# Kernel tuning notes

Hardware: AMD Instinct MI355X
Metric: run time of the kernel (lower is better)

Reference implementation:

```python
import jax, jax.numpy as jnp
import numpy as np
import math

B, S, H, HKV, DH = 2, 2048, 32, 1, 128  # batch, seq, q heads, kv heads, per-head/model dim
D_K = 128


def setup_inputs() -> dict:
    key = jax.random.key(0)
    ks = jax.random.split(key, 11)
    sc = 0.02
    return {
        "query": jax.random.normal(ks[0], (B, S, DH), jnp.float32),
        "key": jax.random.normal(ks[1], (B, S, DH), jnp.float32),
        "values": jax.random.normal(ks[2], (B, S, DH), jnp.float32),
        "W_q": jax.random.normal(ks[3], (DH, H * DH), jnp.float32) * sc,
        "b_q": jnp.zeros((H * DH,), jnp.float32),
        "W_k": jax.random.normal(ks[4], (DH, HKV * DH), jnp.float32) * sc,
        "b_k": jnp.zeros((HKV * DH,), jnp.float32),
        "W_v": jax.random.normal(ks[5], (DH, HKV * DH), jnp.float32) * sc,
        "b_v": jnp.zeros((HKV * DH,), jnp.float32),
        "W_o": jax.random.normal(ks[6], (H * DH, DH), jnp.float32) * sc,
        "b_o": jnp.zeros((DH,), jnp.float32),
    }


def reference(query, key, values, W_q, b_q, W_k, b_k, W_v, b_v, W_o, b_o):
    # Projections (note: the original uses raw .view(-1, H, S, DH), which we
    # replicate exactly — it is a reshape, not a transpose).
    q = (query @ W_q + b_q).reshape(-1, H, S, DH)      # [B,H,S,DH]
    k = (key @ W_k + b_k).reshape(-1, HKV, S, DH)       # [B,1,S,DH]
    v = (values @ W_v + b_v).reshape(-1, HKV, S, DH)    # [B,1,S,DH]

    # RoPE outputs in the original forward are computed but never used
    # (dead code), and mask defaults to None -> no masking. Dropout omitted
    # for deterministic reference.
    scores = jnp.matmul(q, jnp.swapaxes(k, -1, -2)) / math.sqrt(D_K)  # [B,H,S,S]
    attn = jax.nn.softmax(scores, axis=-1)
    out = jnp.matmul(attn, v)                           # [B,H,S,DH]
    out = jnp.swapaxes(out, 1, 2).reshape(-1, S, H * DH)
    return out @ W_o + b_o                              # [B,S,DH]
```

## Files before the change

### kernel.cpp

```cpp
#include <hip/hip_runtime.h>
#include <hip/hip_bf16.h>
#include <math.h>


typedef __hip_bfloat16 bf16;
typedef __attribute__((ext_vector_type(8))) short short8;
typedef __attribute__((ext_vector_type(4))) float floatx4;

static constexpr int B_ = 2;
static constexpr int S_ = 2048;
static constexpr int H_ = 32;
static constexpr int DH_ = 128;

#define GL16(gp, lp)                                              \
  __builtin_amdgcn_global_load_lds(                               \
      (const __attribute__((address_space(1))) void*)(gp),        \
      (__attribute__((address_space(3))) void*)(lp), 16, 0, 0)

__global__ void detect_dtype(const unsigned short* __restrict__ q,
                             int* __restrict__ flag) {
  int t = threadIdx.x;
  int cnt = 0;
#pragma unroll
  for (int i = 0; i < 8; ++i) {
    unsigned short u = q[t * 8 + i];
    int e = (u >> 7) & 0xFF;
    if (e < 0x60) cnt++;
  }
#pragma unroll
  for (int off = 1; off < 64; off <<= 1) cnt += __shfl_xor(cnt, off);
  if (t == 0) *flag = (cnt >= 8) ? 1 : 0;
}

__global__ void cvt3_bf16(const void* __restrict__ a, const void* __restrict__ b,
                          const void* __restrict__ c, bf16* __restrict__ da,
                          bf16* __restrict__ db, bf16* __restrict__ dc, int n,
                          const int* __restrict__ flag) {
  int i = blockIdx.x * 256 + threadIdx.x;
  if (i >= n) return;
  const void* s = (blockIdx.y == 0) ? a : (blockIdx.y == 1) ? b : c;
  bf16* d = (blockIdx.y == 0) ? da : (blockIdx.y == 1) ? db : dc;
  d[i] = (*flag) ? __float2bfloat16(((const float*)s)[i]) : ((const bf16*)s)[i];
}

__global__ void cvt_biases(const void* __restrict__ bq, const void* __restrict__ bk,
                           const void* __restrict__ bv, const void* __restrict__ bo,
                           float* __restrict__ fq, float* __restrict__ fk,
                           float* __restrict__ fv, float* __restrict__ fo,
                           const int* __restrict__ flag, float qscale) {
  int i = blockIdx.x * 256 + threadIdx.x;
  const void* s;
  float* d;
  int off;
  float sc = 1.f;
  if (i < 4096) { s = bq; d = fq; off = i; sc = qscale; }
  else if (i < 4224) { s = bk; d = fk; off = i - 4096; }
  else if (i < 4352) { s = bv; d = fv; off = i - 4224; }
  else if (i < 4480) { s = bo; d = fo; off = i - 4352; }
  else return;
  float v = (*flag) ? ((const float*)s)[off]
                    : __bfloat162float(((const bf16*)s)[off]);
  d[off] = v * sc;
}

__global__ void ttranspose(const void* __restrict__ W, bf16* __restrict__ Wt,
                           int K, int N, const int* __restrict__ flag,
                           float scale) {
  __shared__ bf16 tile[64][66];
  int n0 = blockIdx.x * 64, k0 = blockIdx.y * 64;
  int c = threadIdx.x & 63;
  int r4 = threadIdx.x >> 6;
  bool f = (*flag) != 0;
#pragma unroll
  for (int i = 0; i < 16; ++i) {
    int r = r4 * 16 + i;
    float v = f ? ((const float*)W)[(size_t)(k0 + r) * N + n0 + c]
                : __bfloat162float(((const bf16*)W)[(size_t)(k0 + r) * N + n0 + c]);
    tile[r][c] = __float2bfloat16(v * scale);
  }
  __syncthreads();
#pragma unroll
  for (int i = 0; i < 16; ++i) {
    int cc = r4 * 16 + i;
    Wt[(size_t)(n0 + cc) * K + k0 + c] = tile[c][cc];
  }
}

template <int MODE>
__global__ __launch_bounds__(256) void gemm2(
    const bf16* __restrict__ A, int lda, const bf16* __restrict__ Bt, int ldb,
    const float* __restrict__ bias, bf16* __restrict__ Cb,
    float* __restrict__ Cf, int K_len, int ldc) {
  const int lane = threadIdx.x & 63;
  const int wave = threadIdx.x >> 6;
  const int lm = lane & 15;
  const int quad = lane >> 4;
  const int row_base = blockIdx.y * 64 + wave * 16;
  const int col_base = blockIdx.x * 64;
  const int koff = blockIdx.z * K_len;

  const bf16* arow = A + (size_t)(row_base + lm) * lda + koff + quad * 8;
  const bf16* brow = Bt + (size_t)(col_base + lm) * ldb + koff + quad * 8;

  floatx4 z = {0.f, 0.f, 0.f, 0.f};
  floatx4 acc[4] = {z, z, z, z};

  for (int kk = 0; kk < K_len; kk += 32) {
    short8 a = *(const short8*)(arow + kk);
#pragma unroll
    for (int t = 0; t < 4; ++t) {
      short8 b = *(const short8*)(brow + (size_t)(t * 16) * ldb + kk);
      acc[t] = __builtin_amdgcn_mfma_f32_16x16x32_bf16(a, b, acc[t], 0, 0, 0);
    }
  }

#pragma unroll
  for (int t = 0; t < 4; ++t) {
    int col = col_base + t * 16 + lm;
#pragma unroll
    for (int r = 0; r < 4; ++r) {
      int row = row_base + quad * 4 + r;
      if (MODE == 0) {
        Cb[(size_t)row * ldc + col] = __float2bfloat16(acc[t][r] + bias[col]);
      } else if (MODE == 3) {
        Cb[((size_t)((row >> 11) * DH_ + col)) * S_ + (row & 2047)] =
            __float2bfloat16(acc[t][r] + bias[col]);
      } else {
        Cf[(size_t)blockIdx.z * (4096 * 128) + (size_t)row * ldc + col] =
            acc[t][r];
      }
    }
  }
}

__global__ void finish_out(const float* __restrict__ parts,
                           const float* __restrict__ bias,
                           float* __restrict__ out) {
  int i = blockIdx.x * 256 + threadIdx.x;
  const float4* p = (const float4*)parts;
  float4 a = p[i];
  float4 b = p[i + 131072];
  float4 c = p[i + 262144];
  float4 d = p[i + 393216];
  float4 bb = ((const float4*)bias)[i & 31];
  float4 o;
  o.x = a.x + b.x + c.x + d.x + bb.x;
  o.y = a.y + b.y + c.y + d.y + bb.y;
  o.z = a.z + b.z + c.z + d.z + bb.z;
  o.w = a.w + b.w + c.w + d.w + bb.w;
  ((float4*)out)[i] = o;
}

static __device__ __forceinline__ unsigned bpack(float lo, float hi) {
  unsigned a = __float_as_uint(lo) + 0x8000u;
  unsigned b = __float_as_uint(hi) + 0x8000u;
  return __builtin_amdgcn_perm(b, a, 0x07060302u);
}

static __device__ __forceinline__ float fexp2(float x) {
#if __has_builtin(__builtin_amdgcn_exp2f)
  return __builtin_amdgcn_exp2f(x);
#else
  return exp2f(x);
#endif
}

static __device__ __forceinline__ void pexchange(const unsigned pk[8],
                                                 int quad, short8* pf) {
  const bool q0 = (quad & 1);
  unsigned sA0 = q0 ? pk[0] : pk[2];
  unsigned sA1 = q0 ? pk[1] : pk[3];
  unsigned sA2 = q0 ? pk[4] : pk[6];
  unsigned sA3 = q0 ? pk[5] : pk[7];
  unsigned r0 = (unsigned)__shfl_xor((int)sA0, 16);
  unsigned r1 = (unsigned)__shfl_xor((int)sA1, 16);
  unsigned r2 = (unsigned)__shfl_xor((int)sA2, 16);
  unsigned r3 = (unsigned)__shfl_xor((int)sA3, 16);
  unsigned M0 = q0 ? r0 : pk[0];
  unsigned M1 = q0 ? r1 : pk[1];
  unsigned M2 = q0 ? pk[2] : r0;
  unsigned M3 = q0 ? pk[3] : r1;
  unsigned M4 = q0 ? r2 : pk[4];
  unsigned M5 = q0 ? r3 : pk[5];
  unsigned M6 = q0 ? pk[6] : r2;
  unsigned M7 = q0 ? pk[7] : r3;
  const bool swp = (quad == 1) || (quad == 2);
  union { unsigned u[4]; short8 v; } f0, f1;
  unsigned t0, t1;
  t0 = (unsigned)__shfl_xor((int)M0, 48); f0.u[0] = swp ? t0 : M0;
  t1 = (unsigned)__shfl_xor((int)M1, 48); f0.u[1] = swp ? t1 : M1;
  t0 = (unsigned)__shfl_xor((int)M2, 48); f0.u[2] = swp ? t0 : M2;
  t1 = (unsigned)__shfl_xor((int)M3, 48); f0.u[3] = swp ? t1 : M3;
  t0 = (unsigned)__shfl_xor((int)M4, 48); f1.u[0] = swp ? t0 : M4;
  t1 = (unsigned)__shfl_xor((int)M5, 48); f1.u[1] = swp ? t1 : M5;
  t0 = (unsigned)__shfl_xor((int)M6, 48); f1.u[2] = swp ? t0 : M6;
  t1 = (unsigned)__shfl_xor((int)M7, 48); f1.u[3] = swp ? t1 : M7;
  pf[0] = f0.v;
  pf[1] = f1.v;
}

__global__ __launch_bounds__(256, 2) void flash_attn(
    const bf16* __restrict__ Qp, const bf16* __restrict__ Kp,
    const bf16* __restrict__ Vt, bf16* __restrict__ O2c) {
  const int tid = threadIdx.x;
  const int lane = tid & 63;
  const int wave = tid >> 6;
  const int lm = lane & 15;
  const int quad = lane >> 4;
  const int qt = blockIdx.x;
  const int h = blockIdx.y;
  const int b = blockIdx.z;

  __shared__ __align__(16) bf16 Klds[2][64 * 128];
  __shared__ __align__(16) bf16 Vlds[2][128 * 64];

  const int base = qt * 128 + wave * 32;
  const bf16* qrow = Qp + ((size_t)b * S_ + h * 64 + (base >> 5)) * 4096;
  short8 qf0[4], qf1[4];
#pragma unroll
  for (int ks = 0; ks < 4; ++ks) {
    qf0[ks] = *(const short8*)(qrow + lm * 128 + quad * 8 + ks * 32);
    qf1[ks] = *(const short8*)(qrow + (16 + lm) * 128 + quad * 8 + ks * 32);
  }

  const bf16* Kb = Kp + (size_t)b * S_ * DH_;
  const bf16* Vb = Vt + (size_t)b * DH_ * S_;
  const int sw = lm & 7;

  const bf16* kgp[4];
  const bf16* vgp[4];
#pragma unroll
  for (int i = 0; i < 4; ++i) {
    const int inst = wave * 4 + i;
    const int krow = inst * 4 + quad;
    kgp[i] = Kb + (size_t)krow * 128 + ((lm ^ (krow & 7)) * 8);
    const int vrow = inst * 8 + (lane >> 3);
    vgp[i] = Vb + (size_t)vrow * S_ + (((lane & 7) ^ (vrow & 7)) * 8);
  }

  floatx4 z = {0.f, 0.f, 0.f, 0.f};
  floatx4 oa0[8], oa1[8];
#pragma unroll
  for (int nt = 0; nt < 8; ++nt) { oa0[nt] = z; oa1[nt] = z; }
  float ls0 = 0.f, ls1 = 0.f;

#pragma unroll
  for (int i = 0; i < 4; ++i) {
    GL16(kgp[i], &Klds[0][(wave * 4 + i) * 512]);
    GL16(vgp[i], &Vlds[0][(wave * 4 + i) * 512]);
    kgp[i] += 64 * 128;
    vgp[i] += 64;
  }
  __syncthreads();

  int cur = 0;
  for (int kb = 0; kb < S_; kb += 64) {
    const bf16* Kc = Klds[cur];
    const bf16* Vc = Vlds[cur];
    if (kb + 64 < S_) {
      bf16* Kn = Klds[cur ^ 1];
      bf16* Vn = Vlds[cur ^ 1];
#pragma unroll
      for (int i = 0; i < 4; ++i) {
        GL16(kgp[i], Kn + (wave * 4 + i) * 512);
        GL16(vgp[i], Vn + (wave * 4 + i) * 512);
        kgp[i] += 64 * 128;
        vgp[i] += 64;
      }
    }

    floatx4 s0[4] = {z, z, z, z}, s1[4] = {z, z, z, z};
    __builtin_amdgcn_s_setprio(1);
#pragma unroll
    for (int t = 0; t < 4; ++t) {
#pragma unroll
      for (int ks = 0; ks < 4; ++ks) {
        short8 kf = *(const short8*)(&Kc[(t * 16 + lm) * 128 +
                                         (((quad + 4 * ks) ^ sw) * 8)]);
        s0[t] = __builtin_amdgcn_mfma_f32_16x16x32_bf16(kf, qf0[ks], s0[t],
                                                        0, 0, 0);
        s1[t] = __builtin_amdgcn_mfma_f32_16x16x32_bf16(kf, qf1[ks], s1[t],
                                                        0, 0, 0);
      }
    }
    __builtin_amdgcn_s_setprio(0);

    unsigned pk0[8], pk1[8];
#pragma unroll
    for (int t = 0; t < 4; ++t) {
      float a0 = fexp2(s0[t][0]), a1 = fexp2(s0[t][1]);
      float a2 = fexp2(s0[t][2]), a3 = fexp2(s0[t][3]);
      ls0 += (a0 + a1) + (a2 + a3);
      pk0[2 * t] = bpack(a0, a1);
      pk0[2 * t + 1] = bpack(a2, a3);
      float c0 = fexp2(s1[t][0]), c1 = fexp2(s1[t][1]);
      float c2 = fexp2(s1[t][2]), c3 = fexp2(s1[t][3]);
      ls1 += (c0 + c1) + (c2 + c3);
      pk1[2 * t] = bpack(c0, c1);
      pk1[2 * t + 1] = bpack(c2, c3);
    }
    short8 pf0[2], pf1[2];
    pexchange(pk0, quad, pf0);
    pexchange(pk1, quad, pf1);

    __builtin_amdgcn_s_setprio(1);
#pragma unroll
    for (int ks2 = 0; ks2 < 2; ++ks2) {
#pragma unroll
      for (int nt = 0; nt < 8; ++nt) {
        short8 vf = *(const short8*)(&Vc[(nt * 16 + lm) * 64 +
                                         (((quad + 4 * ks2) ^ sw) * 8)]);
        oa0[nt] = __builtin_amdgcn_mfma_f32_16x16x32_bf16(pf0[ks2], vf,
                                                          oa0[nt], 0, 0, 0);
        oa1[nt] = __builtin_amdgcn_mfma_f32_16x16x32_bf16(pf1[ks2], vf,
                                                          oa1[nt], 0, 0, 0);
      }
    }
    __builtin_amdgcn_s_setprio(0);
    __syncthreads();
    cur ^= 1;
  }

  ls0 += __shfl_xor(ls0, 16);
  ls0 += __shfl_xor(ls0, 32);
  ls1 += __shfl_xor(ls1, 16);
  ls1 += __shfl_xor(ls1, 32);
  float inv0[4], inv1[4];
#pragma unroll
  for (int r = 0; r < 4; ++r) {
    inv0[r] = 1.0f / __shfl(ls0, quad * 4 + r);
    inv1[r] = 1.0f / __shfl(ls1, quad * 4 + r);
  }

#pragma unroll
  for (int r = 0; r < 4; ++r) {
    int s2a = base + quad * 4 + r;
    int s2b = s2a + 16;
    size_t ba = ((size_t)b * S_ + s2a) * 4096 + (size_t)h * 128;
    size_t bb = ((size_t)b * S_ + s2b) * 4096 + (size_t)h * 128;
#pragma unroll
    for (int nt = 0; nt < 8; ++nt) {
      O2c[ba + nt * 16 + lm] = __float2bfloat16(oa0[nt][r] * inv0[r]);
      O2c[bb + nt * 16 + lm] = __float2bfloat16(oa1[nt][r] * inv1[r]);
    }
  }
}

extern "C" void kernel_launch(void* const* d_in, const int* in_sizes, int n_in,
                              void* d_out, int out_size, void* d_ws,
                              size_t ws_size, hipStream_t stream) {
  (void)in_sizes;
  (void)n_in;
  (void)out_size;
  (void)ws_size;

  const void* query = d_in[0];
  const void* key = d_in[1];
  const void* values = d_in[2];
  const void* W_q = d_in[3];
  const void* b_q = d_in[4];
  const void* W_k = d_in[5];
  const void* b_k = d_in[6];
  const void* W_v = d_in[7];
  const void* b_v = d_in[8];
  const void* W_o = d_in[9];
  const void* b_o = d_in[10];
  float* out = (float*)d_out;

  const float kScale = 0.1275174388204085f;
  const int M = B_ * S_;
  const int QN = B_ * S_ * DH_;

  char* w = (char*)d_ws;
  auto carve = [&](size_t bytes) -> char* {
    char* p = w;
    w += (bytes + 255) & ~(size_t)255;
    return p;
  };
  int* flag = (int*)carve(4);
  bf16* cQ = (bf16*)carve((size_t)QN * 2);
  bf16* cK = (bf16*)carve((size_t)QN * 2);
  bf16* cV = (bf16*)carve((size_t)QN * 2);
  float* fbq = (float*)carve((size_t)H_ * DH_ * 4);
  float* fbk = (float*)carve((size_t)DH_ * 4);
  float* fbv = (float*)carve((size_t)DH_ * 4);
  float* fbo = (float*)carve((size_t)DH_ * 4);
  bf16* Wqt = (bf16*)carve((size_t)DH_ * H_ * DH_ * 2);
  bf16* Wkt = (bf16*)carve((size_t)DH_ * DH_ * 2);
  bf16* Wvt = (bf16*)carve((size_t)DH_ * DH_ * 2);
  bf16* Wot = (bf16*)carve((size_t)H_ * DH_ * DH_ * 2);
  bf16* Kp = (bf16*)carve((size_t)B_ * S_ * DH_ * 2);
  bf16* Vtp = (bf16*)carve((size_t)B_ * S_ * DH_ * 2);
  bf16* Qp = (bf16*)carve((size_t)M * H_ * DH_ * 2);
  bf16* O2c = (bf16*)carve((size_t)M * H_ * DH_ * 2);

  float* parts = (float*)Qp;

  detect_dtype<<<1, 64, 0, stream>>>((const unsigned short*)query, flag);
  cvt3_bf16<<<dim3(QN / 256, 3), 256, 0, stream>>>(query, key, values, cQ, cK,
                                                   cV, QN, flag);
  cvt_biases<<<18, 256, 0, stream>>>(b_q, b_k, b_v, b_o, fbq, fbk, fbv, fbo,
                                     flag, kScale);

  ttranspose<<<dim3(H_ * DH_ / 64, DH_ / 64), 256, 0, stream>>>(
      W_q, Wqt, DH_, H_ * DH_, flag, kScale);
  ttranspose<<<dim3(DH_ / 64, DH_ / 64), 256, 0, stream>>>(W_k, Wkt, DH_, DH_,
                                                           flag, 1.0f);
  ttranspose<<<dim3(DH_ / 64, DH_ / 64), 256, 0, stream>>>(W_v, Wvt, DH_, DH_,
                                                           flag, 1.0f);
  ttranspose<<<dim3(DH_ / 64, H_ * DH_ / 64), 256, 0, stream>>>(
      W_o, Wot, H_ * DH_, DH_, flag, 1.0f);

  gemm2<0><<<dim3(2, 64), 256, 0, stream>>>(cK, DH_, Wkt, DH_, fbk, Kp,
                                            nullptr, DH_, DH_);
  gemm2<3><<<dim3(2, 64), 256, 0, stream>>>(cV, DH_, Wvt, DH_, fbv, Vtp,
                                            nullptr, DH_, 0);
  gemm2<0><<<dim3(64, 64), 256, 0, stream>>>(cQ, DH_, Wqt, DH_, fbq, Qp,
                                             nullptr, DH_, H_ * DH_);

  flash_attn<<<dim3(S_ / 128, H_, B_), 256, 0, stream>>>(Qp, Kp, Vtp, O2c);

  gemm2<4><<<dim3(DH_ / 64, M / 64, 4), 256, 0, stream>>>(
      O2c, H_ * DH_, Wot, H_ * DH_, nullptr, nullptr, parts,
      (H_ * DH_) / 4, DH_);

  finish_out<<<QN / 4 / 256, 256, 0, stream>>>(parts, fbo, out);
}
```

Measured before the change: 363.5 us.

## Merge prep kernels, fuse QKV GEMMs, single-buffer LDS in flash attention

Fuses the conversion, bias and four weight-transpose kernels into one launch, and the three QKV projection GEMMs into one grid, to cut launch count and tail effects. In flash attention, the K/V double buffer becomes a single LDS buffer and launch bounds go from 2 to 4 blocks per CU to raise occupancy. The loads for the next tile are now issued only after compute finishes, so global-to-LDS transfers no longer overlap with MFMA work inside a block and must be hidden by the other resident blocks.

```diff
diff --git a/kernel.cpp b/kernel.cpp
--- a/kernel.cpp
+++ b/kernel.cpp
@@ -32,45 +32,13 @@
   if (t == 0) *flag = (cnt >= 8) ? 1 : 0;
 }
 
-__global__ void cvt3_bf16(const void* __restrict__ a, const void* __restrict__ b,
-                          const void* __restrict__ c, bf16* __restrict__ da,
-                          bf16* __restrict__ db, bf16* __restrict__ dc, int n,
-                          const int* __restrict__ flag) {
-  int i = blockIdx.x * 256 + threadIdx.x;
-  if (i >= n) return;
-  const void* s = (blockIdx.y == 0) ? a : (blockIdx.y == 1) ? b : c;
-  bf16* d = (blockIdx.y == 0) ? da : (blockIdx.y == 1) ? db : dc;
-  d[i] = (*flag) ? __float2bfloat16(((const float*)s)[i]) : ((const bf16*)s)[i];
-}
-
-__global__ void cvt_biases(const void* __restrict__ bq, const void* __restrict__ bk,
-                           const void* __restrict__ bv, const void* __restrict__ bo,
-                           float* __restrict__ fq, float* __restrict__ fk,
-                           float* __restrict__ fv, float* __restrict__ fo,
-                           const int* __restrict__ flag, float qscale) {
-  int i = blockIdx.x * 256 + threadIdx.x;
-  const void* s;
-  float* d;
-  int off;
-  float sc = 1.f;
-  if (i < 4096) { s = bq; d = fq; off = i; sc = qscale; }
-  else if (i < 4224) { s = bk; d = fk; off = i - 4096; }
-  else if (i < 4352) { s = bv; d = fv; off = i - 4224; }
-  else if (i < 4480) { s = bo; d = fo; off = i - 4352; }
-  else return;
-  float v = (*flag) ? ((const float*)s)[off]
-                    : __bfloat162float(((const bf16*)s)[off]);
-  d[off] = v * sc;
-}
-
-__global__ void ttranspose(const void* __restrict__ W, bf16* __restrict__ Wt,
-                           int K, int N, const int* __restrict__ flag,
-                           float scale) {
-  __shared__ bf16 tile[64][66];
-  int n0 = blockIdx.x * 64, k0 = blockIdx.y * 64;
+static __device__ void do_ttranspose(const void* __restrict__ W,
+                                     bf16* __restrict__ Wt, int K, int N,
+                                     bool f, float scale, int bx, int by,
+                                     bf16 (*tile)[66]) {
+  int n0 = bx * 64, k0 = by * 64;
   int c = threadIdx.x & 63;
   int r4 = threadIdx.x >> 6;
-  bool f = (*flag) != 0;
 #pragma unroll
   for (int i = 0; i < 16; ++i) {
     int r = r4 * 16 + i;
@@ -86,11 +54,106 @@
   }
 }
 
-template <int MODE>
-__global__ __launch_bounds__(256) void gemm2(
-    const bf16* __restrict__ A, int lda, const bf16* __restrict__ Bt, int ldb,
-    const float* __restrict__ bias, bf16* __restrict__ Cb,
-    float* __restrict__ Cf, int K_len, int ldc) {
+__global__ void prep(const void* __restrict__ query, const void* __restrict__ key,
+                     const void* __restrict__ values, bf16* __restrict__ cQ,
+                     bf16* __restrict__ cK, bf16* __restrict__ cV,
+                     const void* __restrict__ bq, const void* __restrict__ bk,
+                     const void* __restrict__ bv, const void* __restrict__ bo,
+                     float* __restrict__ fbq, float* __restrict__ fbk,
+                     float* __restrict__ fbv, float* __restrict__ fbo,
+                     const void* __restrict__ Wq, bf16* __restrict__ Wqt,
+                     const void* __restrict__ Wk, bf16* __restrict__ Wkt,
+                     const void* __restrict__ Wv, bf16* __restrict__ Wvt,
+                     const void* __restrict__ Wo, bf16* __restrict__ Wot,
+                     const int* __restrict__ flag, float qscale) {
+  __shared__ bf16 tile[64][66];
+  const int id = blockIdx.x;
+  const bool f = (*flag) != 0;
+  if (id < 6144) {
+    int y = id >> 11, x = id & 2047;
+    int i = x * 256 + threadIdx.x;
+    const void* s = (y == 0) ? query : (y == 1) ? key : values;
+    bf16* d = (y == 0) ? cQ : (y == 1) ? cK : cV;
+    d[i] = f ? __float2bfloat16(((const float*)s)[i]) : ((const bf16*)s)[i];
+  } else if (id < 6162) {
+    int i = (id - 6144) * 256 + threadIdx.x;
+    const void* s; float* d; int off; float sc = 1.f;
+    if (i < 4096) { s = bq; d = fbq; off = i; sc = qscale; }
+    else if (i < 4224) { s = bk; d = fbk; off = i - 4096; }
+    else if (i < 4352) { s = bv; d = fbv; off = i - 4224; }
+    else if (i < 4480) { s = bo; d = fbo; off = i - 4352; }
+    else return;
+    float v = f ? ((const float*)s)[off]
+                : __bfloat162float(((const bf16*)s)[off]);
+    d[off] = v * sc;
+  } else if (id < 6290) {
+    int j = id - 6162;
+    do_ttranspose(Wq, Wqt, DH_, H_ * DH_, f, qscale, j % 64, j / 64, tile);
+  } else if (id < 6294) {
+    int j = id - 6290;
+    do_ttranspose(Wk, Wkt, DH_, DH_, f, 1.0f, j % 2, j / 2, tile);
+  } else if (id < 6298) {
+    int j = id - 6294;
+    do_ttranspose(Wv, Wvt, DH_, DH_, f, 1.0f, j % 2, j / 2, tile);
+  } else {
+    int j = id - 6298;
+    do_ttranspose(Wo, Wot, H_ * DH_, DH_, f, 1.0f, j % 2, j / 2, tile);
+  }
+}
+
+__global__ __launch_bounds__(256) void gemm_qkv(
+    const bf16* __restrict__ cQ, const bf16* __restrict__ cK,
+    const bf16* __restrict__ cV, const bf16* __restrict__ Wqt,
+    const bf16* __restrict__ Wkt, const bf16* __restrict__ Wvt,
+    const float* __restrict__ fbq, const float* __restrict__ fbk,
+    const float* __restrict__ fbv, bf16* __restrict__ Qp,
+    bf16* __restrict__ Kp, bf16* __restrict__ Vtp) {
+  const int bx = blockIdx.x;
+  const bf16* A; const bf16* Bt; const float* bias; bf16* Cb;
+  int mode, ldc, colb;
+  if (bx < 64)      { A = cQ; Bt = Wqt; bias = fbq; Cb = Qp;  mode = 0; ldc = 4096; colb = bx; }
+  else if (bx < 66) { A = cK; Bt = Wkt; bias = fbk; Cb = Kp;  mode = 0; ldc = 128;  colb = bx - 64; }
+  else              { A = cV; Bt = Wvt; bias = fbv; Cb = Vtp; mode = 3; ldc = 0;    colb = bx - 66; }
+
+  const int lane = threadIdx.x & 63;
+  const int wave = threadIdx.x >> 6;
+  const int lm = lane & 15;
+  const int quad = lane >> 4;
+  const int row_base = blockIdx.y * 64 + wave * 16;
+  const int col_base = colb * 64;
+
+  const bf16* arow = A + (size_t)(row_base + lm) * DH_ + quad * 8;
+  const bf16* brow = Bt + (size_t)(col_base + lm) * DH_ + quad * 8;
+
+  floatx4 z = {0.f, 0.f, 0.f, 0.f};
+  floatx4 acc[4] = {z, z, z, z};
+  for (int kk = 0; kk < DH_; kk += 32) {
+    short8 a = *(const short8*)(arow + kk);
+#pragma unroll
+    for (int t = 0; t < 4; ++t) {
+      short8 b = *(const short8*)(brow + (size_t)(t * 16) * DH_ + kk);
+      acc[t] = __builtin_amdgcn_mfma_f32_16x16x32_bf16(a, b, acc[t], 0, 0, 0);
+    }
+  }
+#pragma unroll
+  for (int t = 0; t < 4; ++t) {
+    int col = col_base + t * 16 + lm;
+#pragma unroll
+    for (int r = 0; r < 4; ++r) {
+      int row = row_base + quad * 4 + r;
+      if (mode == 0) {
+        Cb[(size_t)row * ldc + col] = __float2bfloat16(acc[t][r] + bias[col]);
+      } else {
+        Cb[((size_t)((row >> 11) * DH_ + col)) * S_ + (row & 2047)] =
+            __float2bfloat16(acc[t][r] + bias[col]);
+      }
+    }
+  }
+}
+
+__global__ __launch_bounds__(256) void gemm_out(
+    const bf16* __restrict__ A, const bf16* __restrict__ Bt,
+    float* __restrict__ Cf, int K_len) {
   const int lane = threadIdx.x & 63;
   const int wave = threadIdx.x >> 6;
   const int lm = lane & 15;
@@ -99,36 +162,27 @@
   const int col_base = blockIdx.x * 64;
   const int koff = blockIdx.z * K_len;
 
-  const bf16* arow = A + (size_t)(row_base + lm) * lda + koff + quad * 8;
-  const bf16* brow = Bt + (size_t)(col_base + lm) * ldb + koff + quad * 8;
+  const bf16* arow = A + (size_t)(row_base + lm) * (H_ * DH_) + koff + quad * 8;
+  const bf16* brow = Bt + (size_t)(col_base + lm) * (H_ * DH_) + koff + quad * 8;
 
   floatx4 z = {0.f, 0.f, 0.f, 0.f};
   floatx4 acc[4] = {z, z, z, z};
-
   for (int kk = 0; kk < K_len; kk += 32) {
     short8 a = *(const short8*)(arow + kk);
 #pragma unroll
     for (int t = 0; t < 4; ++t) {
-      short8 b = *(const short8*)(brow + (size_t)(t * 16) * ldb + kk);
+      short8 b = *(const short8*)(brow + (size_t)(t * 16) * (H_ * DH_) + kk);
       acc[t] = __builtin_amdgcn_mfma_f32_16x16x32_bf16(a, b, acc[t], 0, 0, 0);
     }
   }
-
 #pragma unroll
   for (int t = 0; t < 4; ++t) {
     int col = col_base + t * 16 + lm;
 #pragma unroll
     for (int r = 0; r < 4; ++r) {
       int row = row_base + quad * 4 + r;
-      if (MODE == 0) {
-        Cb[(size_t)row * ldc + col] = __float2bfloat16(acc[t][r] + bias[col]);
-      } else if (MODE == 3) {
-        Cb[((size_t)((row >> 11) * DH_ + col)) * S_ + (row & 2047)] =
-            __float2bfloat16(acc[t][r] + bias[col]);
-      } else {
-        Cf[(size_t)blockIdx.z * (4096 * 128) + (size_t)row * ldc + col] =
-            acc[t][r];
-      }
+      Cf[(size_t)blockIdx.z * (4096 * 128) + (size_t)row * DH_ + col] =
+          acc[t][r];
     }
   }
 }
@@ -199,7 +253,7 @@
   pf[1] = f1.v;
 }
 
-__global__ __launch_bounds__(256, 2) void flash_attn(
+__global__ __launch_bounds__(256, 4) void flash_attn(
     const bf16* __restrict__ Qp, const bf16* __restrict__ Kp,
     const bf16* __restrict__ Vt, bf16* __restrict__ O2c) {
   const int tid = threadIdx.x;
@@ -211,8 +265,8 @@
   const int h = blockIdx.y;
   const int b = blockIdx.z;
 
-  __shared__ __align__(16) bf16 Klds[2][64 * 128];
-  __shared__ __align__(16) bf16 Vlds[2][128 * 64];
+  __shared__ __align__(16) bf16 Klds[64 * 128];
+  __shared__ __align__(16) bf16 Vlds[128 * 64];
 
   const int base = qt * 128 + wave * 32;
   const bf16* qrow = Qp + ((size_t)b * S_ + h * 64 + (base >> 5)) * 4096;
@@ -246,28 +300,14 @@
 
 #pragma unroll
   for (int i = 0; i < 4; ++i) {
-    GL16(kgp[i], &Klds[0][(wave * 4 + i) * 512]);
-    GL16(vgp[i], &Vlds[0][(wave * 4 + i) * 512]);
+    GL16(kgp[i], &Klds[(wave * 4 + i) * 512]);
+    GL16(vgp[i], &Vlds[(wave * 4 + i) * 512]);
     kgp[i] += 64 * 128;
     vgp[i] += 64;
   }
-  __syncthreads();
-
-  int cur = 0;
+
   for (int kb = 0; kb < S_; kb += 64) {
-    const bf16* Kc = Klds[cur];
-    const bf16* Vc = Vlds[cur];
-    if (kb + 64 < S_) {
-      bf16* Kn = Klds[cur ^ 1];
-      bf16* Vn = Vlds[cur ^ 1];
-#pragma unroll
-      for (int i = 0; i < 4; ++i) {
-        GL16(kgp[i], Kn + (wave * 4 + i) * 512);
-        GL16(vgp[i], Vn + (wave * 4 + i) * 512);
-        kgp[i] += 64 * 128;
-        vgp[i] += 64;
-      }
-    }
+    __syncthreads();
 
     floatx4 s0[4] = {z, z, z, z}, s1[4] = {z, z, z, z};
     __builtin_amdgcn_s_setprio(1);
@@ -275,8 +315,8 @@
     for (int t = 0; t < 4; ++t) {
 #pragma unroll
       for (int ks = 0; ks < 4; ++ks) {
-        short8 kf = *(const short8*)(&Kc[(t * 16 + lm) * 128 +
-                                         (((quad + 4 * ks) ^ sw) * 8)]);
+        short8 kf = *(const short8*)(&Klds[(t * 16 + lm) * 128 +
+                                           (((quad + 4 * ks) ^ sw) * 8)]);
         s0[t] = __builtin_amdgcn_mfma_f32_16x16x32_bf16(kf, qf0[ks], s0[t],
                                                         0, 0, 0);
         s1[t] = __builtin_amdgcn_mfma_f32_16x16x32_bf16(kf, qf1[ks], s1[t],
@@ -308,8 +348,8 @@
     for (int ks2 = 0; ks2 < 2; ++ks2) {
 #pragma unroll
       for (int nt = 0; nt < 8; ++nt) {
-        short8 vf = *(const short8*)(&Vc[(nt * 16 + lm) * 64 +
-                                         (((quad + 4 * ks2) ^ sw) * 8)]);
+        short8 vf = *(const short8*)(&Vlds[(nt * 16 + lm) * 64 +
+                                           (((quad + 4 * ks2) ^ sw) * 8)]);
         oa0[nt] = __builtin_amdgcn_mfma_f32_16x16x32_bf16(pf0[ks2], vf,
                                                           oa0[nt], 0, 0, 0);
         oa1[nt] = __builtin_amdgcn_mfma_f32_16x16x32_bf16(pf1[ks2], vf,
@@ -318,7 +358,16 @@
     }
     __builtin_amdgcn_s_setprio(0);
     __syncthreads();
-    cur ^= 1;
+
+    if (kb + 64 < S_) {
+#pragma unroll
+      for (int i = 0; i < 4; ++i) {
+        GL16(kgp[i], &Klds[(wave * 4 + i) * 512]);
+        GL16(vgp[i], &Vlds[(wave * 4 + i) * 512]);
+        kgp[i] += 64 * 128;
+        vgp[i] += 64;
+      }
+    }
   }
 
   ls0 += __shfl_xor(ls0, 16);
@@ -397,32 +446,18 @@
   float* parts = (float*)Qp;
 
   detect_dtype<<<1, 64, 0, stream>>>((const unsigned short*)query, flag);
-  cvt3_bf16<<<dim3(QN / 256, 3), 256, 0, stream>>>(query, key, values, cQ, cK,
-                                                   cV, QN, flag);
-  cvt_biases<<<18, 256, 0, stream>>>(b_q, b_k, b_v, b_o, fbq, fbk, fbv, fbo,
-                                     flag, kScale);
-
-  ttranspose<<<dim3(H_ * DH_ / 64, DH_ / 64), 256, 0, stream>>>(
-      W_q, Wqt, DH_, H_ * DH_, flag, kScale);
-  ttranspose<<<dim3(DH_ / 64, DH_ / 64), 256, 0, stream>>>(W_k, Wkt, DH_, DH_,
-                                                           flag, 1.0f);
-  ttranspose<<<dim3(DH_ / 64, DH_ / 64), 256, 0, stream>>>(W_v, Wvt, DH_, DH_,
-                                                           flag, 1.0f);
-  ttranspose<<<dim3(DH_ / 64, H_ * DH_ / 64), 256, 0, stream>>>(
-      W_o, Wot, H_ * DH_, DH_, flag, 1.0f);
-
-  gemm2<0><<<dim3(2, 64), 256, 0, stream>>>(cK, DH_, Wkt, DH_, fbk, Kp,
-                                            nullptr, DH_, DH_);
-  gemm2<3><<<dim3(2, 64), 256, 0, stream>>>(cV, DH_, Wvt, DH_, fbv, Vtp,
-                                            nullptr, DH_, 0);
-  gemm2<0><<<dim3(64, 64), 256, 0, stream>>>(cQ, DH_, Wqt, DH_, fbq, Qp,
-                                             nullptr, DH_, H_ * DH_);
+
+  prep<<<6426, 256, 0, stream>>>(query, key, values, cQ, cK, cV, b_q, b_k,
+                                 b_v, b_o, fbq, fbk, fbv, fbo, W_q, Wqt, W_k,
+                                 Wkt, W_v, Wvt, W_o, Wot, flag, kScale);
+
+  gemm_qkv<<<dim3(68, 64), 256, 0, stream>>>(cQ, cK, cV, Wqt, Wkt, Wvt, fbq,
+                                             fbk, fbv, Qp, Kp, Vtp);
 
   flash_attn<<<dim3(S_ / 128, H_, B_), 256, 0, stream>>>(Qp, Kp, Vtp, O2c);
 
-  gemm2<4><<<dim3(DH_ / 64, M / 64, 4), 256, 0, stream>>>(
-      O2c, H_ * DH_, Wot, H_ * DH_, nullptr, nullptr, parts,
-      (H_ * DH_) / 4, DH_);
+  gemm_out<<<dim3(DH_ / 64, M / 64, 4), 256, 0, stream>>>(
+      O2c, Wot, parts, (H_ * DH_) / 4);
 
   finish_out<<<QN / 4 / 256, 256, 0, stream>>>(parts, fbo, out);
 }
```

Result: slower. 680.8 us (+87.3%).
